# Kernel optimization log

Measured on AMD Instinct MI355X. Metric: run time of the kernel, lower is better.

The kernel has to match this reference:

```python
import jax, jax.numpy as jnp
import numpy as np

NUM_DEM = 2
VOCAB = 10000
EMB = 128


def setup_inputs() -> dict:
    key = jax.random.key(0)
    k_src, k_emb, k_w1, k_w2 = jax.random.split(key, 4)
    B = 16384
    # 0/1 multi-hot style input (demographic cols also 0/1; math identical)
    src = jax.random.randint(k_src, (B, NUM_DEM + VOCAB), 0, 2).astype(jnp.float32)
    embed = jax.random.normal(k_emb, (VOCAB, EMB), dtype=jnp.float32)
    W1 = jax.random.normal(k_w1, (NUM_DEM + EMB, 16), dtype=jnp.float32) * 0.1
    b1 = jnp.full((16,), 0.01, dtype=jnp.float32)
    W2 = jax.random.normal(k_w2, (16, 2), dtype=jnp.float32) * 0.1
    b2 = jnp.full((2,), 0.01, dtype=jnp.float32)
    return {"src": src, "embed": embed, "W1": W1, "b1": b1, "W2": W2, "b2": b2}


def reference(src, embed, W1, b1, W2, b2):
    dem = src[:, :NUM_DEM]                         # [B, 2]
    codes = src[:, NUM_DEM:].astype(jnp.int32)     # [B, V]
    mask = (codes != 0).astype(embed.dtype)        # multi-hot indicator [B, V]
    counts = jnp.sum(mask, axis=1, keepdims=True)  # [B, 1]
    # fused multi-hot gather + mean pooling (embedding-bag mean)
    pooled = (mask @ embed) / counts               # [B, EMB]
    x = jnp.concatenate([dem, pooled], axis=1)     # [B, 2+EMB]
    h = jnp.tanh(x @ W1 + b1)
    return h @ W2 + b2                             # [B, 2]
```

## Files before the change

### kernel.cpp

```cpp
#include <hip/hip_runtime.h>

#define NUM_DEM 2
#define VOCAB 10000
#define EMB 128
#define NROWS 16384
#define ROWLEN (NUM_DEM + VOCAB)
#define KSTEPS 313
#define PCOLS 132
#define BPACK_USHORTS (KSTEPS * 4096)
#define BPACK_BYTES (BPACK_USHORTS * 2)

typedef float f32x4 __attribute__((ext_vector_type(4)));
typedef __bf16 bf16x8 __attribute__((ext_vector_type(8)));
typedef short s16x8 __attribute__((ext_vector_type(8)));

union Frag {
    s16x8 s;
    bf16x8 b;
    unsigned int u[4];
    unsigned short h[8];
};

__device__ __forceinline__ unsigned short f2bf_rtne(float f) {
    unsigned int u = __float_as_uint(f);
    u += 0x7FFFu + ((u >> 16) & 1u);
    return (unsigned short)(u >> 16);
}

__global__ void pack_embed_k(const float* __restrict__ embed,
                             unsigned short* __restrict__ bp) {
    int id = blockIdx.x * blockDim.x + threadIdx.x;
    if (id >= KSTEPS * 8 * 64) return;
    int l = id & 63;
    int c = (id >> 6) & 7;
    int t = id >> 9;
    int kbase = t * 32 + ((l >> 4) * 8);
    int n = c * 16 + (l & 15);
    unsigned short v[8];
#pragma unroll
    for (int j = 0; j < 8; ++j) {
        int k = kbase + j;
        float f = (k < VOCAB) ? embed[(size_t)k * EMB + n] : 0.0f;
        v[j] = f2bf_rtne(f);
    }
    uint4 w;
    w.x = (unsigned int)v[0] | ((unsigned int)v[1] << 16);
    w.y = (unsigned int)v[2] | ((unsigned int)v[3] << 16);
    w.z = (unsigned int)v[4] | ((unsigned int)v[5] << 16);
    w.w = (unsigned int)v[6] | ((unsigned int)v[7] << 16);
    *reinterpret_cast<uint4*>(bp + (size_t)id * 8) = w;
}

typedef const __attribute__((address_space(1))) unsigned int* gas_u32p;
typedef __attribute__((address_space(3))) unsigned int* las_u32p;
#define GLOAD_LDS16(g, l)                                                              \
    __builtin_amdgcn_global_load_lds((gas_u32p)(g), (las_u32p)(l), 16, 0, 0)

__global__ __launch_bounds__(256, 4) void main_gemm_k(
    const float* __restrict__ src, const unsigned short* __restrict__ bp,
    float* __restrict__ part, int nch) {
    __shared__ alignas(16) unsigned short ldsB[2 * 4096];

    const int tid = threadIdx.x;
    const int lane = tid & 63;
    const int wid = tid >> 6;
    const int rb = blockIdx.x & 255;
    const int ch = blockIdx.x >> 8;
    const int t0 = (KSTEPS * ch) / nch;
    const int t1 = (KSTEPS * (ch + 1)) / nch;

    const int rowbase = rb * 64 + wid * 16;
    const int arow = rowbase + (lane & 15);
    const int kgrp8 = (lane >> 4) * 8;
    const float* asrc = src + (size_t)arow * ROWLEN + NUM_DEM + kgrp8;

    f32x4 pacc[8];
#pragma unroll
    for (int f = 0; f < 8; ++f) pacc[f] = (f32x4){0.f, 0.f, 0.f, 0.f};
    f32x4 cacc = (f32x4){0.f, 0.f, 0.f, 0.f};

    Frag onesf;
    {
        unsigned short o = ((lane & 15) == 0) ? (unsigned short)0x3F80 : (unsigned short)0;
        unsigned int ow = (unsigned int)o | ((unsigned int)o << 16);
        onesf.u[0] = ow; onesf.u[1] = ow; onesf.u[2] = ow; onesf.u[3] = ow;
    }

    int t = t0;
    for (; t + 2 <= t1; t += 2) {
        const unsigned short* gB0 = bp + (size_t)t * 4096 + wid * 1024 + lane * 8;
        const unsigned short* gB1 = gB0 + 4096;
        unsigned short* lB0 = ldsB + wid * 1024 + lane * 8;
        unsigned short* lB1 = lB0 + 4096;
        GLOAD_LDS16(gB0, lB0);
        GLOAD_LDS16(gB0 + 512, lB0 + 512);
        GLOAD_LDS16(gB1, lB1);
        GLOAD_LDS16(gB1 + 512, lB1 + 512);

        f32x4 z = (f32x4){0.f, 0.f, 0.f, 0.f};
        f32x4 a00 = z, a01 = z, a10 = z, a11 = z;
        if (t * 32 + kgrp8 + 8 <= VOCAB) {
            const f32x4* ap = reinterpret_cast<const f32x4*>(asrc + (size_t)t * 32);
            a00 = ap[0];
            a01 = ap[1];
        }
        if ((t + 1) * 32 + kgrp8 + 8 <= VOCAB) {
            const f32x4* ap = reinterpret_cast<const f32x4*>(asrc + (size_t)(t + 1) * 32);
            a10 = ap[0];
            a11 = ap[1];
        }

        __syncthreads();

        Frag af0, af1;
        af0.u[0] = __builtin_amdgcn_perm(__float_as_uint(a00.y), __float_as_uint(a00.x), 0x07060302u);
        af0.u[1] = __builtin_amdgcn_perm(__float_as_uint(a00.w), __float_as_uint(a00.z), 0x07060302u);
        af0.u[2] = __builtin_amdgcn_perm(__float_as_uint(a01.y), __float_as_uint(a01.x), 0x07060302u);
        af0.u[3] = __builtin_amdgcn_perm(__float_as_uint(a01.w), __float_as_uint(a01.z), 0x07060302u);
        af1.u[0] = __builtin_amdgcn_perm(__float_as_uint(a10.y), __float_as_uint(a10.x), 0x07060302u);
        af1.u[1] = __builtin_amdgcn_perm(__float_as_uint(a10.w), __float_as_uint(a10.z), 0x07060302u);
        af1.u[2] = __builtin_amdgcn_perm(__float_as_uint(a11.y), __float_as_uint(a11.x), 0x07060302u);
        af1.u[3] = __builtin_amdgcn_perm(__float_as_uint(a11.w), __float_as_uint(a11.z), 0x07060302u);

#pragma unroll
        for (int f = 0; f < 8; ++f) {
            Frag bfr;
            bfr.s = *reinterpret_cast<const s16x8*>(ldsB + f * 512 + lane * 8);
            pacc[f] = __builtin_amdgcn_mfma_f32_16x16x32_bf16(af0.b, bfr.b, pacc[f], 0, 0, 0);
        }
        cacc = __builtin_amdgcn_mfma_f32_16x16x32_bf16(af0.b, onesf.b, cacc, 0, 0, 0);
#pragma unroll
        for (int f = 0; f < 8; ++f) {
            Frag bfr;
            bfr.s = *reinterpret_cast<const s16x8*>(ldsB + 4096 + f * 512 + lane * 8);
            pacc[f] = __builtin_amdgcn_mfma_f32_16x16x32_bf16(af1.b, bfr.b, pacc[f], 0, 0, 0);
        }
        cacc = __builtin_amdgcn_mfma_f32_16x16x32_bf16(af1.b, onesf.b, cacc, 0, 0, 0);

        __syncthreads();
    }
    if (t < t1) {
        const unsigned short* gB0 = bp + (size_t)t * 4096 + wid * 1024 + lane * 8;
        unsigned short* lB0 = ldsB + wid * 1024 + lane * 8;
        GLOAD_LDS16(gB0, lB0);
        GLOAD_LDS16(gB0 + 512, lB0 + 512);

        f32x4 z = (f32x4){0.f, 0.f, 0.f, 0.f};
        f32x4 a00 = z, a01 = z;
        if (t * 32 + kgrp8 + 8 <= VOCAB) {
            const f32x4* ap = reinterpret_cast<const f32x4*>(asrc + (size_t)t * 32);
            a00 = ap[0];
            a01 = ap[1];
        }
        __syncthreads();
        Frag af0;
        af0.u[0] = __builtin_amdgcn_perm(__float_as_uint(a00.y), __float_as_uint(a00.x), 0x07060302u);
        af0.u[1] = __builtin_amdgcn_perm(__float_as_uint(a00.w), __float_as_uint(a00.z), 0x07060302u);
        af0.u[2] = __builtin_amdgcn_perm(__float_as_uint(a01.y), __float_as_uint(a01.x), 0x07060302u);
        af0.u[3] = __builtin_amdgcn_perm(__float_as_uint(a01.w), __float_as_uint(a01.z), 0x07060302u);
#pragma unroll
        for (int f = 0; f < 8; ++f) {
            Frag bfr;
            bfr.s = *reinterpret_cast<const s16x8*>(ldsB + f * 512 + lane * 8);
            pacc[f] = __builtin_amdgcn_mfma_f32_16x16x32_bf16(af0.b, bfr.b, pacc[f], 0, 0, 0);
        }
        cacc = __builtin_amdgcn_mfma_f32_16x16x32_bf16(af0.b, onesf.b, cacc, 0, 0, 0);
        __syncthreads();
    }

    const int rlo = (lane >> 4) * 4;
    float* pch = part + (size_t)ch * NROWS * PCOLS;
#pragma unroll
    for (int f = 0; f < 8; ++f) {
#pragma unroll
        for (int r = 0; r < 4; ++r) {
            int row = rowbase + rlo + r;
            pch[(size_t)row * PCOLS + f * 16 + (lane & 15)] = pacc[f][r];
        }
    }
    if ((lane & 15) == 0) {
#pragma unroll
        for (int r = 0; r < 4; ++r) {
            int row = rowbase + rlo + r;
            pch[(size_t)row * PCOLS + 128] = cacc[r];
        }
    }
}

__global__ __launch_bounds__(256) void mlp_k(const float* __restrict__ part,
                                             const float* __restrict__ src,
                                             const float* __restrict__ W1,
                                             const float* __restrict__ b1,
                                             const float* __restrict__ W2,
                                             const float* __restrict__ b2,
                                             float* __restrict__ out, int nch) {
    __shared__ float xls[16][131];
    __shared__ float hls[16][16];
    __shared__ float cnt[16];
    const int tid = threadIdx.x;
    const int rb = blockIdx.x * 16;

    if (tid < 16) {
        float s = 0.f;
        for (int c = 0; c < nch; ++c)
            s += part[((size_t)c * NROWS + rb + tid) * PCOLS + 128];
        cnt[tid] = s;
    }
    if (tid >= 16 && tid < 48) {
        int r = (tid - 16) >> 1, d = (tid - 16) & 1;
        xls[r][d] = src[(size_t)(rb + r) * ROWLEN + d];
    }
    __syncthreads();

    for (int idx = tid; idx < 16 * 128; idx += 256) {
        int r = idx >> 7, col = idx & 127;
        float s = 0.f;
        for (int c = 0; c < nch; ++c)
            s += part[((size_t)c * NROWS + rb + r) * PCOLS + col];
        xls[r][NUM_DEM + col] = s / cnt[r];
    }
    __syncthreads();

    {
        int r = tid >> 4, u = tid & 15;
        float acc = b1[u];
        for (int i = 0; i < NUM_DEM + EMB; ++i) acc += xls[r][i] * W1[i * 16 + u];
        hls[r][u] = tanhf(acc);
    }
    __syncthreads();

    if (tid < 32) {
        int r = tid >> 1, o = tid & 1;
        float acc = b2[o];
#pragma unroll
        for (int u = 0; u < 16; ++u) acc += hls[r][u] * W2[u * 2 + o];
        out[(size_t)(rb + r) * 2 + o] = acc;
    }
}

extern "C" void kernel_launch(void* const* d_in, const int* in_sizes, int n_in,
                              void* d_out, int out_size, void* d_ws, size_t ws_size,
                              hipStream_t stream) {
    const float* src = (const float*)d_in[0];
    const float* embed = (const float*)d_in[1];
    const float* W1 = (const float*)d_in[2];
    const float* b1 = (const float*)d_in[3];
    const float* W2 = (const float*)d_in[4];
    const float* b2 = (const float*)d_in[5];
    float* out = (float*)d_out;

    unsigned short* bpack = (unsigned short*)d_ws;
    float* part = (float*)((char*)d_ws + BPACK_BYTES);

    const size_t part1 = (size_t)NROWS * PCOLS * sizeof(float);
    int nch = 4;
    while (nch > 1 && BPACK_BYTES + part1 * (size_t)nch > ws_size) nch >>= 1;

    hipLaunchKernelGGL(pack_embed_k, dim3((KSTEPS * 8 * 64 + 255) / 256), dim3(256), 0,
                       stream, embed, bpack);
    hipLaunchKernelGGL(main_gemm_k, dim3(256 * nch), dim3(256), 0, stream, src, bpack,
                       part, nch);
    hipLaunchKernelGGL(mlp_k, dim3(NROWS / 16), dim3(256), 0, stream, part, src, W1, b1,
                       W2, b2, out, nch);
}
```

Before: 203.4 us.

## Pre-pack multi-hot input into bitmasks before the embedding GEMM

Adds a streaming kernel that reads the fp32 multi-hot input once and packs each 8-element group into a byte, laid out per 16-row group to match the MFMA A-fragment order. The main GEMM then loads one 16-bit mask word per two k-steps and expands the bits into bf16 ones and zeros in registers, instead of loading 32 bytes of fp32 per lane per step. This frees the GEMM loop from the heavy global A traffic and its latency, so the large read can run as a pure bandwidth-bound pass. The price is an extra kernel launch, an extra small write and read of the mask buffer, and more workspace use.

```diff
diff --git a/kernel.cpp b/kernel.cpp
--- a/kernel.cpp
+++ b/kernel.cpp
@@ -8,7 +8,11 @@
 #define KSTEPS 313
 #define PCOLS 132
 #define BPACK_USHORTS (KSTEPS * 4096)
-#define BPACK_BYTES (BPACK_USHORTS * 2)
+#define BPACK_BYTES ((size_t)BPACK_USHORTS * 2)
+#define NRG (NROWS / 16)
+#define MK_I 158
+#define MK_BYTES ((size_t)NRG * MK_I * 128)
+#define NCH 4
 
 typedef float f32x4 __attribute__((ext_vector_type(4)));
 typedef __bf16 bf16x8 __attribute__((ext_vector_type(8)));
@@ -51,13 +55,50 @@
     *reinterpret_cast<uint4*>(bp + (size_t)id * 8) = w;
 }
 
+__global__ __launch_bounds__(256) void mask_pack_k(const float* __restrict__ src,
+                                                   unsigned char* __restrict__ mk) {
+    const int b = blockIdx.x;
+    const int rg = b >> 1, kh = b & 1;
+    const int tid = threadIdx.x;
+    const int r16 = tid >> 4, j = tid & 15;
+    const int row = rg * 16 + r16;
+    const float* srow = src + (size_t)row * ROWLEN + NUM_DEM;
+    const int ldst = ((j & 3) << 4) | r16;
+    const int w0 = kh ? 40 : 0, w1 = kh ? 79 : 40;
+    unsigned char* mkrg = mk + (size_t)rg * MK_I * 128;
+    for (int w = w0; w < w1; ++w) {
+        const int k0 = w * 128 + j * 8;
+        unsigned int byte = 0;
+        if (k0 + 8 <= VOCAB) {
+            const f32x4* ap = reinterpret_cast<const f32x4*>(srow + k0);
+            f32x4 f0 = ap[0], f1 = ap[1];
+#pragma unroll
+            for (int jj = 0; jj < 4; ++jj) {
+                byte |= (f0[jj] != 0.0f) ? (1u << jj) : 0u;
+                byte |= (f1[jj] != 0.0f) ? (1u << (jj + 4)) : 0u;
+            }
+        }
+        const int s = w * 4 + (j >> 2);
+        mkrg[(size_t)(s >> 1) * 128 + ldst * 2 + (s & 1)] = (unsigned char)byte;
+    }
+}
+
 typedef const __attribute__((address_space(1))) unsigned int* gas_u32p;
 typedef __attribute__((address_space(3))) unsigned int* las_u32p;
 #define GLOAD_LDS16(g, l)                                                              \
     __builtin_amdgcn_global_load_lds((gas_u32p)(g), (las_u32p)(l), 16, 0, 0)
 
+__device__ __forceinline__ void expand_byte(unsigned int b, Frag& af) {
+#pragma unroll
+    for (int p = 0; p < 4; ++p) {
+        unsigned int lo = ((b >> (2 * p)) & 1u) ? 0x3F800000u : 0u;
+        unsigned int hi = ((b >> (2 * p + 1)) & 1u) ? 0x3F800000u : 0u;
+        af.u[p] = (lo >> 16) | hi;
+    }
+}
+
 __global__ __launch_bounds__(256, 4) void main_gemm_k(
-    const float* __restrict__ src, const unsigned short* __restrict__ bp,
+    const unsigned char* __restrict__ mk, const unsigned short* __restrict__ bp,
     float* __restrict__ part, int nch) {
     __shared__ alignas(16) unsigned short ldsB[2 * 4096];
 
@@ -70,9 +111,8 @@
     const int t1 = (KSTEPS * (ch + 1)) / nch;
 
     const int rowbase = rb * 64 + wid * 16;
-    const int arow = rowbase + (lane & 15);
-    const int kgrp8 = (lane >> 4) * 8;
-    const float* asrc = src + (size_t)arow * ROWLEN + NUM_DEM + kgrp8;
+    const int rgw = rb * 4 + wid;
+    const unsigned char* mrow = mk + (size_t)rgw * MK_I * 128 + lane * 2;
 
     f32x4 pacc[8];
 #pragma unroll
@@ -97,30 +137,13 @@
         GLOAD_LDS16(gB1, lB1);
         GLOAD_LDS16(gB1 + 512, lB1 + 512);
 
-        f32x4 z = (f32x4){0.f, 0.f, 0.f, 0.f};
-        f32x4 a00 = z, a01 = z, a10 = z, a11 = z;
-        if (t * 32 + kgrp8 + 8 <= VOCAB) {
-            const f32x4* ap = reinterpret_cast<const f32x4*>(asrc + (size_t)t * 32);
-            a00 = ap[0];
-            a01 = ap[1];
-        }
-        if ((t + 1) * 32 + kgrp8 + 8 <= VOCAB) {
-            const f32x4* ap = reinterpret_cast<const f32x4*>(asrc + (size_t)(t + 1) * 32);
-            a10 = ap[0];
-            a11 = ap[1];
-        }
-
-        __syncthreads();
-
+        unsigned short m =
+            *reinterpret_cast<const unsigned short*>(mrow + (size_t)(t >> 1) * 128);
         Frag af0, af1;
-        af0.u[0] = __builtin_amdgcn_perm(__float_as_uint(a00.y), __float_as_uint(a00.x), 0x07060302u);
-        af0.u[1] = __builtin_amdgcn_perm(__float_as_uint(a00.w), __float_as_uint(a00.z), 0x07060302u);
-        af0.u[2] = __builtin_amdgcn_perm(__float_as_uint(a01.y), __float_as_uint(a01.x), 0x07060302u);
-        af0.u[3] = __builtin_amdgcn_perm(__float_as_uint(a01.w), __float_as_uint(a01.z), 0x07060302u);
-        af1.u[0] = __builtin_amdgcn_perm(__float_as_uint(a10.y), __float_as_uint(a10.x), 0x07060302u);
-        af1.u[1] = __builtin_amdgcn_perm(__float_as_uint(a10.w), __float_as_uint(a10.z), 0x07060302u);
-        af1.u[2] = __builtin_amdgcn_perm(__float_as_uint(a11.y), __float_as_uint(a11.x), 0x07060302u);
-        af1.u[3] = __builtin_amdgcn_perm(__float_as_uint(a11.w), __float_as_uint(a11.z), 0x07060302u);
+        expand_byte(m & 0xFFu, af0);
+        expand_byte((unsigned int)m >> 8, af1);
+
+        __syncthreads();
 
 #pragma unroll
         for (int f = 0; f < 8; ++f) {
@@ -145,19 +168,11 @@
         GLOAD_LDS16(gB0, lB0);
         GLOAD_LDS16(gB0 + 512, lB0 + 512);
 
-        f32x4 z = (f32x4){0.f, 0.f, 0.f, 0.f};
-        f32x4 a00 = z, a01 = z;
-        if (t * 32 + kgrp8 + 8 <= VOCAB) {
-            const f32x4* ap = reinterpret_cast<const f32x4*>(asrc + (size_t)t * 32);
-            a00 = ap[0];
-            a01 = ap[1];
-        }
-        __syncthreads();
+        unsigned short m =
+            *reinterpret_cast<const unsigned short*>(mrow + (size_t)(t >> 1) * 128);
         Frag af0;
-        af0.u[0] = __builtin_amdgcn_perm(__float_as_uint(a00.y), __float_as_uint(a00.x), 0x07060302u);
-        af0.u[1] = __builtin_amdgcn_perm(__float_as_uint(a00.w), __float_as_uint(a00.z), 0x07060302u);
-        af0.u[2] = __builtin_amdgcn_perm(__float_as_uint(a01.y), __float_as_uint(a01.x), 0x07060302u);
-        af0.u[3] = __builtin_amdgcn_perm(__float_as_uint(a01.w), __float_as_uint(a01.z), 0x07060302u);
+        expand_byte(m & 0xFFu, af0);
+        __syncthreads();
 #pragma unroll
         for (int f = 0; f < 8; ++f) {
             Frag bfr;
@@ -250,15 +265,17 @@
     float* out = (float*)d_out;
 
     unsigned short* bpack = (unsigned short*)d_ws;
-    float* part = (float*)((char*)d_ws + BPACK_BYTES);
+    unsigned char* mk = (unsigned char*)d_ws + BPACK_BYTES;
+    float* part = (float*)((char*)d_ws + BPACK_BYTES + MK_BYTES);
 
     const size_t part1 = (size_t)NROWS * PCOLS * sizeof(float);
-    int nch = 4;
-    while (nch > 1 && BPACK_BYTES + part1 * (size_t)nch > ws_size) nch >>= 1;
+    int nch = NCH;
+    while (nch > 1 && BPACK_BYTES + MK_BYTES + part1 * (size_t)nch > ws_size) nch >>= 1;
 
     hipLaunchKernelGGL(pack_embed_k, dim3((KSTEPS * 8 * 64 + 255) / 256), dim3(256), 0,
                        stream, embed, bpack);
-    hipLaunchKernelGGL(main_gemm_k, dim3(256 * nch), dim3(256), 0, stream, src, bpack,
+    hipLaunchKernelGGL(mask_pack_k, dim3(NRG * 2), dim3(256), 0, stream, src, mk);
+    hipLaunchKernelGGL(main_gemm_k, dim3(256 * nch), dim3(256), 0, stream, mk, bpack,
                        part, nch);
     hipLaunchKernelGGL(mlp_k, dim3(NROWS / 16), dim3(256), 0, stream, part, src, W1, b1,
                        W2, b2, out, nch);
```

Measured after the change: 240.4 us. +18.2%, slower.
